# Kernel optimization log

Measured on AMD Instinct MI355X. Metric: run time of the kernel, lower is better.

## Reference

```python
import jax, jax.numpy as jnp
import numpy as np

N = 50000       # nodes
E = 800000      # edges (before self-loops)
F_IN = 128
HID = 64
HEADS = 4
OUT_DIM = 128
N_CLS = 2
NG = 500        # num graphs
SLOPE = 0.2     # GATConv leaky_relu negative slope
EPS = 1e-5      # BatchNorm eps


def setup_inputs() -> dict:
    key = jax.random.key(0)
    ks = jax.random.split(key, 24)
    s = 0.05
    d = {
        "x": jax.random.normal(ks[0], (N, F_IN), jnp.float32),
        "edge_index": jax.random.randint(ks[1], (2, E), 0, N, jnp.int64),
        "batch": jnp.sort(jax.random.randint(ks[2], (N,), 0, NG, jnp.int64)),
        # GATConv 1
        "W1": jax.random.normal(ks[3], (F_IN, HEADS * HID), jnp.float32) * s,
        "att_src1": jax.random.normal(ks[4], (HEADS, HID), jnp.float32) * s,
        "att_dst1": jax.random.normal(ks[5], (HEADS, HID), jnp.float32) * s,
        "b1": jnp.zeros((HEADS * HID,), jnp.float32),
        # BN1 (eval mode)
        "g1": jnp.ones((HEADS * HID,), jnp.float32),
        "be1": jnp.zeros((HEADS * HID,), jnp.float32),
        "rm1": jnp.zeros((HEADS * HID,), jnp.float32),
        "rv1": jnp.ones((HEADS * HID,), jnp.float32),
        # GATConv 2
        "W2": jax.random.normal(ks[6], (HEADS * HID, HEADS * HID), jnp.float32) * s,
        "att_src2": jax.random.normal(ks[7], (HEADS, HID), jnp.float32) * s,
        "att_dst2": jax.random.normal(ks[8], (HEADS, HID), jnp.float32) * s,
        "b2": jnp.zeros((HEADS * HID,), jnp.float32),
        # BN2 (eval mode)
        "g2": jnp.ones((HEADS * HID,), jnp.float32),
        "be2": jnp.zeros((HEADS * HID,), jnp.float32),
        "rm2": jnp.zeros((HEADS * HID,), jnp.float32),
        "rv2": jnp.ones((HEADS * HID,), jnp.float32),
        # MLP head
        "lw1": jax.random.normal(ks[9], (HEADS * HID, OUT_DIM), jnp.float32) * s,
        "lb1": jnp.zeros((OUT_DIM,), jnp.float32),
        "lw2": jax.random.normal(ks[10], (OUT_DIM, N_CLS), jnp.float32) * s,
        "lb2": jnp.zeros((N_CLS,), jnp.float32),
    }
    return d


def _gat_conv(x, src, dst, W, a_src, a_dst, b):
    """PyG GATConv (concat heads, add_self_loops=True, eval -> no dropout)."""
    n = x.shape[0]
    h = (x @ W).reshape(n, HEADS, -1)            # [N, H, C]
    loop = jnp.arange(n)
    s = jnp.concatenate([src, loop])             # self-loops appended
    d = jnp.concatenate([dst, loop])
    a_s = jnp.sum(h * a_src, axis=-1)            # [N, H]
    a_d = jnp.sum(h * a_dst, axis=-1)            # [N, H]
    e = jax.nn.leaky_relu(a_s[s] + a_d[d], SLOPE)   # [Et, H]
    # softmax over incoming edges per destination node
    m = jax.ops.segment_max(e, d, num_segments=n)
    ex = jnp.exp(e - m[d])
    denom = jax.ops.segment_sum(ex, d, num_segments=n)
    alpha = ex / denom[d]                        # [Et, H]
    msg = h[s] * alpha[:, :, None]               # [Et, H, C]
    out = jax.ops.segment_sum(msg, d, num_segments=n)
    return out.reshape(n, -1) + b


def _bn_eval(x, g, be, rm, rv):
    return (x - rm) * jax.lax.rsqrt(rv + EPS) * g + be


def reference(x, edge_index, batch, W1, att_src1, att_dst1, b1, g1, be1, rm1, rv1,
              W2, att_src2, att_dst2, b2, g2, be2, rm2, rv2, lw1, lb1, lw2, lb2):
    src, dst = edge_index[0], edge_index[1]
    h = jax.nn.relu(_gat_conv(x, src, dst, W1, att_src1, att_dst1, b1))
    h = _bn_eval(h, g1, be1, rm1, rv1)
    h = jax.nn.relu(_gat_conv(h, src, dst, W2, att_src2, att_dst2, b2))
    h = _bn_eval(h, g2, be2, rm2, rv2)
    # global mean pool over graphs
    sums = jax.ops.segment_sum(h, batch, num_segments=NG)
    cnt = jax.ops.segment_sum(jnp.ones((h.shape[0],), h.dtype), batch, num_segments=NG)
    pooled = sums / jnp.clip(cnt, 1.0)[:, None]
    z = jax.nn.relu(pooled @ lw1 + lb1)
    return z @ lw2 + lb2
```

## Files before the change

### kernel.cpp

```cpp
#include <hip/hip_runtime.h>
#include <hip/hip_bf16.h>
#include <math.h>

#define N_NODES 50000
#define M_PAD   50048
#define N_EDGES 800000
#define F_IN 128
#define HID 64
#define HEADS 4
#define FEAT 256
#define OUT_DIM 128
#define N_CLS 2
#define NG 500
#define SLOPE 0.2f
#define BN_EPS 1e-5f
#define WCAP 64
#define NCHUNK ((N_NODES + 255) / 256)

typedef __attribute__((ext_vector_type(8))) short short8;
typedef __attribute__((ext_vector_type(4))) float floatx4;
typedef __attribute__((ext_vector_type(2))) float floatx2;

__device__ inline unsigned short f2bf(float f) {
    unsigned int u = __float_as_uint(f);
    unsigned int lsb = (u >> 16) & 1u;
    return (unsigned short)((u + 0x7fffu + lsb) >> 16);
}

template<bool AF32>
__global__ __launch_bounds__(256) void gemm_mfma_gat(
    const void* __restrict__ Av, const unsigned short* __restrict__ BT,
    const float* __restrict__ att_src, const float* __restrict__ att_dst,
    unsigned char* __restrict__ h8, float* __restrict__ a_s,
    float* __restrict__ a_d, int K) {
    constexpr int LS = 40;
    constexpr int C8 = 144;
    __shared__ unsigned short smem[128 * 132];
    unsigned short* As = smem;
    unsigned short* Bs = smem + 128 * LS;
    unsigned char*  s8 = (unsigned char*)smem;
    int t = threadIdx.x;
    int lane = t & 63, w = t >> 6;
    int wm = (w >> 1) * 64, wn = (w & 1) * 64;
    int row0 = blockIdx.y * 128, col0 = blockIdx.x * 128;

    floatx4 acc[4][4] = {};

    int r0 = t >> 2,            c0 = (t & 3) * 8;
    int r1 = (t + 256) >> 2,    c1 = ((t + 256) & 3) * 8;
    int mrow = lane & 15, quad = lane >> 4;

    const unsigned short* Ab = (const unsigned short*)Av;
    const float* Af = (const float*)Av;

    for (int k0 = 0; k0 < K; k0 += 32) {
        if (AF32) {
            uint4 p0 = make_uint4(0, 0, 0, 0), p1 = p0;
            if (row0 + r0 < N_NODES) {
                float4 f0 = *(const float4*)&Af[(long long)(row0 + r0) * K + k0 + c0];
                float4 f1 = *(const float4*)&Af[(long long)(row0 + r0) * K + k0 + c0 + 4];
                p0.x = (unsigned)f2bf(f0.x) | ((unsigned)f2bf(f0.y) << 16);
                p0.y = (unsigned)f2bf(f0.z) | ((unsigned)f2bf(f0.w) << 16);
                p0.z = (unsigned)f2bf(f1.x) | ((unsigned)f2bf(f1.y) << 16);
                p0.w = (unsigned)f2bf(f1.z) | ((unsigned)f2bf(f1.w) << 16);
            }
            if (row0 + r1 < N_NODES) {
                float4 f0 = *(const float4*)&Af[(long long)(row0 + r1) * K + k0 + c1];
                float4 f1 = *(const float4*)&Af[(long long)(row0 + r1) * K + k0 + c1 + 4];
                p1.x = (unsigned)f2bf(f0.x) | ((unsigned)f2bf(f0.y) << 16);
                p1.y = (unsigned)f2bf(f0.z) | ((unsigned)f2bf(f0.w) << 16);
                p1.z = (unsigned)f2bf(f1.x) | ((unsigned)f2bf(f1.y) << 16);
                p1.w = (unsigned)f2bf(f1.z) | ((unsigned)f2bf(f1.w) << 16);
            }
            *(uint4*)&As[r0 * LS + c0] = p0;
            *(uint4*)&As[r1 * LS + c1] = p1;
        } else {
            *(uint4*)&As[r0 * LS + c0] = *(const uint4*)&Ab[(long long)(row0 + r0) * K + k0 + c0];
            *(uint4*)&As[r1 * LS + c1] = *(const uint4*)&Ab[(long long)(row0 + r1) * K + k0 + c1];
        }
        *(uint4*)&Bs[r0 * LS + c0] = *(const uint4*)&BT[(long long)(col0 + r0) * K + k0 + c0];
        *(uint4*)&Bs[r1 * LS + c1] = *(const uint4*)&BT[(long long)(col0 + r1) * K + k0 + c1];
        __syncthreads();
        short8 af[4], bf[4];
        #pragma unroll
        for (int i = 0; i < 4; i++) {
            af[i] = *(const short8*)&As[(wm + i * 16 + mrow) * LS + quad * 8];
            bf[i] = *(const short8*)&Bs[(wn + i * 16 + mrow) * LS + quad * 8];
        }
        #pragma unroll
        for (int mi = 0; mi < 4; mi++)
            #pragma unroll
            for (int ni = 0; ni < 4; ni++)
                acc[mi][ni] = __builtin_amdgcn_mfma_f32_16x16x32_bf16(af[mi], bf[ni],
                                                                      acc[mi][ni], 0, 0, 0);
        __syncthreads();
    }

    int head = blockIdx.x * 2 + (w & 1);
    float ats[4], atd[4];
    #pragma unroll
    for (int ni = 0; ni < 4; ni++) {
        ats[ni] = att_src[head * 64 + ni * 16 + mrow];
        atd[ni] = att_dst[head * 64 + ni * 16 + mrow];
    }
    #pragma unroll
    for (int mi = 0; mi < 4; mi++) {
        #pragma unroll
        for (int r = 0; r < 4; r++) {
            int row = row0 + wm + mi * 16 + quad * 4 + r;
            float ps = 0.f, pd = 0.f;
            #pragma unroll
            for (int ni = 0; ni < 4; ni++) {
                float v = acc[mi][ni][r];
                ps += v * ats[ni];
                pd += v * atd[ni];
            }
            #pragma unroll
            for (int off = 1; off < 16; off <<= 1) {
                ps += __shfl_xor(ps, off);
                pd += __shfl_xor(pd, off);
            }
            if (mrow == 0 && row < N_NODES) {
                a_s[row * 4 + head] = ps;
                a_d[row * 4 + head] = pd;
            }
        }
    }

    #pragma unroll
    for (int mi = 0; mi < 4; mi++)
        #pragma unroll
        for (int r = 0; r < 4; r++) {
            int row = wm + mi * 16 + quad * 4 + r;
            #pragma unroll
            for (int ni = 0; ni < 4; ni += 2) {
                int pk = __builtin_amdgcn_cvt_pk_fp8_f32(acc[mi][ni][r],
                                                         acc[mi][ni + 1][r], 0, false);
                s8[row * C8 + wn + ni * 16 + mrow]       = (unsigned char)(pk & 0xff);
                s8[row * C8 + wn + (ni + 1) * 16 + mrow] = (unsigned char)((pk >> 8) & 0xff);
            }
        }
    __syncthreads();
    {
        int r2 = t >> 1, half = t & 1;
        const uint4* sp = (const uint4*)&s8[r2 * C8 + half * 64];
        uint4* dp = (uint4*)&h8[(long long)(row0 + r2) * FEAT + col0 + half * 64];
        #pragma unroll
        for (int k = 0; k < 4; k++)
            dp[k] = sp[k];
    }
}

__global__ void prep(const float* __restrict__ W1, const float* __restrict__ W2,
                     unsigned short* __restrict__ W1T, unsigned short* __restrict__ W2T,
                     int* __restrict__ deg, unsigned long long* __restrict__ h1bf_pad) {
    int i = blockIdx.x * 256 + threadIdx.x;
    if (i < F_IN * 256) {
        int k = i >> 8, n = i & 255;
        W1T[n * F_IN + k] = f2bf(W1[i]);
    }
    int j = i - F_IN * 256;
    if (j >= 0 && j < FEAT * 256) {
        int k = j >> 8, n = j & 255;
        W2T[n * FEAT + k] = f2bf(W2[j]);
    }
    if (i < N_NODES) deg[i] = 0;
    if (i < (M_PAD - N_NODES) * FEAT / 4) h1bf_pad[i] = 0ULL;
}

__global__ void degree_count(const int* __restrict__ src, const int* __restrict__ dst,
                             int* __restrict__ deg, int* __restrict__ epos) {
    int e = blockIdx.x * blockDim.x + threadIdx.x;
    if (e >= N_EDGES + N_NODES) return;
    int d = (e < N_EDGES) ? dst[e] : (e - N_EDGES);
    epos[e] = atomicAdd(&deg[d], 1);
}

__global__ __launch_bounds__(256) void scan_k1(const int* __restrict__ deg,
                                               int* __restrict__ bsum) {
    int b = blockIdx.x, t = threadIdx.x;
    int i = b * 256 + t;
    int v = (i < N_NODES) ? deg[i] : 0;
    #pragma unroll
    for (int off = 32; off > 0; off >>= 1) v += __shfl_down(v, off);
    __shared__ int ws[4];
    if ((t & 63) == 0) ws[t >> 6] = v;
    __syncthreads();
    if (t == 0) bsum[b] = ws[0] + ws[1] + ws[2] + ws[3];
}

__global__ __launch_bounds__(256) void scan_k2(const int* __restrict__ bsum,
                                               int* __restrict__ boff,
                                               int* __restrict__ row_start) {
    int t = threadIdx.x;
    int lane = t & 63, wid = t >> 6;
    int v = (t < NCHUNK) ? bsum[t] : 0;
    int x = v;
    #pragma unroll
    for (int off = 1; off < 64; off <<= 1) {
        int y = __shfl_up(x, off);
        if (lane >= off) x += y;
    }
    __shared__ int wsum[4], woff[4];
    if (lane == 63) wsum[wid] = x;
    __syncthreads();
    if (t == 0) {
        int s = 0;
        #pragma unroll
        for (int w = 0; w < 4; w++) { int tw = wsum[w]; woff[w] = s; s += tw; }
        row_start[N_NODES] = s;
    }
    __syncthreads();
    if (t < NCHUNK) boff[t] = x - v + woff[wid];
}

__global__ __launch_bounds__(256) void scan_k3(const int* __restrict__ deg,
                                               const int* __restrict__ boff,
                                               int* __restrict__ row_start) {
    int b = blockIdx.x, t = threadIdx.x;
    int lane = t & 63, wid = t >> 6;
    int i = b * 256 + t;
    int v = (i < N_NODES) ? deg[i] : 0;
    int x = v;
    #pragma unroll
    for (int off = 1; off < 64; off <<= 1) {
        int y = __shfl_up(x, off);
        if (lane >= off) x += y;
    }
    __shared__ int wsum[4], woff[4];
    if (lane == 63) wsum[wid] = x;
    __syncthreads();
    if (t == 0) {
        int s = boff[b];
        #pragma unroll
        for (int w = 0; w < 4; w++) { int tw = wsum[w]; woff[w] = s; s += tw; }
    }
    __syncthreads();
    if (i < N_NODES) row_start[i] = x - v + woff[wid];
}

__global__ void scatter_edges(const int* __restrict__ src, const int* __restrict__ dst,
                              const int* __restrict__ row_start, const int* __restrict__ epos,
                              int* __restrict__ csr_src) {
    int e = blockIdx.x * blockDim.x + threadIdx.x;
    if (e >= N_EDGES + N_NODES) return;
    int s, d;
    if (e < N_EDGES) { s = src[e]; d = dst[e]; } else { s = d = e - N_EDGES; }
    csr_src[row_start[d] + epos[e]] = s;
}

__global__ __launch_bounds__(256) void gat_fused(
    const int* __restrict__ row_start, const int* __restrict__ csr_src,
    const float* __restrict__ a_s, const float* __restrict__ a_d,
    const unsigned char* __restrict__ h8, const float* __restrict__ bias,
    const float* __restrict__ g, const float* __restrict__ be,
    const float* __restrict__ rm, const float* __restrict__ rv,
    unsigned short* __restrict__ out16) {
    int t = threadIdx.x;
    int lane = t & 63;
    int w = t >> 6;
    int hd = lane >> 4;
    int d = blockIdx.x * 4 + w;

    __shared__ float p_lds[4 * WCAP * 4];
    __shared__ int   o_lds[4 * WCAP];
    float* pw = &p_lds[w * WCAP * 4];
    int*   ow = &o_lds[w * WCAP];

    const unsigned int* __restrict__ H1 = (const unsigned int*)h8;

    int rs = row_start[d], re = row_start[d + 1];
    int deg = re - rs;
    float4 ad4 = *(const float4*)&a_d[d * 4];

    float m_old = -INFINITY;
    float den = 0.f;
    float4 acc = make_float4(0.f, 0.f, 0.f, 0.f);

    for (int base = 0; base < deg; base += WCAP) {
        int cl = min(WCAP, deg - base);
        float lg[4] = {-INFINITY, -INFINITY, -INFINITY, -INFINITY};
        if (lane < cl) {
            int s = csr_src[rs + base + lane];
            ow[lane] = s * 64;
            float4 as4 = *(const float4*)&a_s[s * 4];
            float e0 = as4.x + ad4.x; lg[0] = e0 > 0.f ? e0 : SLOPE * e0;
            float e1 = as4.y + ad4.y; lg[1] = e1 > 0.f ? e1 : SLOPE * e1;
            float e2 = as4.z + ad4.z; lg[2] = e2 > 0.f ? e2 : SLOPE * e2;
            float e3 = as4.w + ad4.w; lg[3] = e3 > 0.f ? e3 : SLOPE * e3;
        }
        float mm = fmaxf(fmaxf(lg[0], lg[1]), fmaxf(lg[2], lg[3]));
        #pragma unroll
        for (int off = 1; off < 64; off <<= 1) mm = fmaxf(mm, __shfl_xor(mm, off));
        float m_new = fmaxf(m_old, mm);
        float alpha = __expf(m_old - m_new);
        m_old = m_new;
        if (lane < cl) {
            float4 pq;
            pq.x = __expf(lg[0] - m_new);
            pq.y = __expf(lg[1] - m_new);
            pq.z = __expf(lg[2] - m_new);
            pq.w = __expf(lg[3] - m_new);
            *(float4*)&pw[lane * 4] = pq;
        }
        acc.x *= alpha; acc.y *= alpha; acc.z *= alpha; acc.w *= alpha;
        den *= alpha;
        int e = 0;
        for (; e + 1 < cl; e += 2) {
            int oA = ow[e], oB = ow[e + 1];
            float pA = pw[e * 4 + hd], pB = pw[(e + 1) * 4 + hd];
            int uA = (int)H1[oA + lane];
            int uB = (int)H1[oB + lane];
            den += pA + pB;
            floatx2 a0 = __builtin_amdgcn_cvt_pk_f32_fp8(uA, false);
            floatx2 a1 = __builtin_amdgcn_cvt_pk_f32_fp8(uA, true);
            floatx2 b0 = __builtin_amdgcn_cvt_pk_f32_fp8(uB, false);
            floatx2 b1 = __builtin_amdgcn_cvt_pk_f32_fp8(uB, true);
            acc.x += pA * a0.x; acc.y += pA * a0.y;
            acc.z += pA * a1.x; acc.w += pA * a1.y;
            acc.x += pB * b0.x; acc.y += pB * b0.y;
            acc.z += pB * b1.x; acc.w += pB * b1.y;
        }
        if (e < cl) {
            int oA = ow[e];
            float pA = pw[e * 4 + hd];
            int uA = (int)H1[oA + lane];
            den += pA;
            floatx2 a0 = __builtin_amdgcn_cvt_pk_f32_fp8(uA, false);
            floatx2 a1 = __builtin_amdgcn_cvt_pk_f32_fp8(uA, true);
            acc.x += pA * a0.x; acc.y += pA * a0.y;
            acc.z += pA * a1.x; acc.w += pA * a1.y;
        }
    }
    float inv = 1.f / den;
    int c0 = lane * 4;
    float4 bi = *(const float4*)&bias[c0];
    float4 gg = *(const float4*)&g[c0];
    float4 bb = *(const float4*)&be[c0];
    float4 mm4 = *(const float4*)&rm[c0];
    float4 vv = *(const float4*)&rv[c0];
    float v0 = fmaxf(acc.x * inv + bi.x, 0.f);
    float v1 = fmaxf(acc.y * inv + bi.y, 0.f);
    float v2 = fmaxf(acc.z * inv + bi.z, 0.f);
    float v3 = fmaxf(acc.w * inv + bi.w, 0.f);
    v0 = (v0 - mm4.x) * rsqrtf(vv.x + BN_EPS) * gg.x + bb.x;
    v1 = (v1 - mm4.y) * rsqrtf(vv.y + BN_EPS) * gg.y + bb.y;
    v2 = (v2 - mm4.z) * rsqrtf(vv.z + BN_EPS) * gg.z + bb.z;
    v3 = (v3 - mm4.w) * rsqrtf(vv.w + BN_EPS) * gg.w + bb.w;
    unsigned long long o =
        (unsigned long long)f2bf(v0) |
        ((unsigned long long)f2bf(v1) << 16) |
        ((unsigned long long)f2bf(v2) << 32) |
        ((unsigned long long)f2bf(v3) << 48);
    __builtin_nontemporal_store(o, (unsigned long long*)&out16[(long long)d * FEAT + c0]);
}

__global__ __launch_bounds__(256) void head_fused(
    const unsigned short* __restrict__ h2, const int* __restrict__ batch,
    const float* __restrict__ lw1, const float* __restrict__ lb1,
    const float* __restrict__ lw2, const float* __restrict__ lb2,
    float* __restrict__ out) {
    int gph = blockIdx.x;
    int t = threadIdx.x;
    __shared__ float pooled[FEAT];
    __shared__ float zl[OUT_DIM];
    __shared__ int lo_s, hi_s;
    if (t == 0) {
        int lo = 0, hi = N_NODES;
        while (lo < hi) { int mid = (lo + hi) >> 1; if (batch[mid] < gph) lo = mid + 1; else hi = mid; }
        lo_s = lo;
        int lo2 = 0, hi2 = N_NODES;
        while (lo2 < hi2) { int mid = (lo2 + hi2) >> 1; if (batch[mid] < gph + 1) lo2 = mid + 1; else hi2 = mid; }
        hi_s = lo2;
    }
    __syncthreads();
    int lo = lo_s, hi = hi_s;
    float a0 = 0.f, a1 = 0.f, a2 = 0.f, a3 = 0.f;
    int n = lo;
    for (; n + 3 < hi; n += 4) {
        a0 += __uint_as_float((unsigned)h2[(long long)n * FEAT + t] << 16);
        a1 += __uint_as_float((unsigned)h2[(long long)(n + 1) * FEAT + t] << 16);
        a2 += __uint_as_float((unsigned)h2[(long long)(n + 2) * FEAT + t] << 16);
        a3 += __uint_as_float((unsigned)h2[(long long)(n + 3) * FEAT + t] << 16);
    }
    for (; n < hi; n++) a0 += __uint_as_float((unsigned)h2[(long long)n * FEAT + t] << 16);
    float cnt = fmaxf((float)(hi - lo), 1.f);
    pooled[t] = (a0 + a1 + a2 + a3) / cnt;
    __syncthreads();
    int j = t >> 1, kh = t & 1;
    float zp = 0.f;
    #pragma unroll 8
    for (int k = kh * 128; k < kh * 128 + 128; k++)
        zp += pooled[k] * lw1[k * OUT_DIM + j];
    zp += __shfl_xor(zp, 1);
    if (kh == 0) zl[j] = fmaxf(zp + lb1[j], 0.f);
    __syncthreads();
    int w = t >> 6, lane = t & 63;
    if (w < 2) {
        float p = zl[lane] * lw2[lane * 2 + w] + zl[lane + 64] * lw2[(lane + 64) * 2 + w];
        #pragma unroll
        for (int off = 1; off < 64; off <<= 1) p += __shfl_xor(p, off);
        if (lane == 0) out[gph * 2 + w] = p + lb2[w];
    }
}

extern "C" void kernel_launch(void* const* d_in, const int* in_sizes, int n_in,
                              void* d_out, int out_size, void* d_ws, size_t ws_size,
                              hipStream_t stream) {
    const float* x       = (const float*)d_in[0];
    const int*   ei      = (const int*)d_in[1];
    const int*   batch   = (const int*)d_in[2];
    const float* W1      = (const float*)d_in[3];
    const float* att_s1  = (const float*)d_in[4];
    const float* att_d1  = (const float*)d_in[5];
    const float* b1      = (const float*)d_in[6];
    const float* g1      = (const float*)d_in[7];
    const float* be1     = (const float*)d_in[8];
    const float* rm1     = (const float*)d_in[9];
    const float* rv1     = (const float*)d_in[10];
    const float* W2      = (const float*)d_in[11];
    const float* att_s2  = (const float*)d_in[12];
    const float* att_d2  = (const float*)d_in[13];
    const float* b2      = (const float*)d_in[14];
    const float* g2      = (const float*)d_in[15];
    const float* be2     = (const float*)d_in[16];
    const float* rm2     = (const float*)d_in[17];
    const float* rv2     = (const float*)d_in[18];
    const float* lw1     = (const float*)d_in[19];
    const float* lb1     = (const float*)d_in[20];
    const float* lw2     = (const float*)d_in[21];
    const float* lb2     = (const float*)d_in[22];
    float* out           = (float*)d_out;

    const int* src = ei;
    const int* dst = ei + N_EDGES;

    char* p = (char*)d_ws;
    auto carve = [&p](size_t bytes) -> void* {
        void* r = (void*)p;
        p += (bytes + 63) & ~(size_t)63;
        return r;
    };
    unsigned short* h2bf = (unsigned short*)carve(sizeof(short) * (size_t)N_NODES * FEAT);
    float* a_s    = (float*)carve(sizeof(float) * N_NODES * HEADS);
    float* a_d    = (float*)carve(sizeof(float) * N_NODES * HEADS);
    int*   deg    = (int*)carve(sizeof(int) * N_NODES);
    int*   epos   = (int*)carve(sizeof(int) * (N_EDGES + N_NODES));
    int*   csr    = (int*)carve(sizeof(int) * (N_EDGES + N_NODES));
    int*   rstart = (int*)carve(sizeof(int) * (N_NODES + 4));
    int*   bsum   = (int*)carve(sizeof(int) * 256);
    int*   boff   = (int*)carve(sizeof(int) * 256);
    unsigned char*  h8   = (unsigned char*)carve((size_t)M_PAD * FEAT);
    unsigned short* h1bf = (unsigned short*)carve(sizeof(short) * (size_t)M_PAD * FEAT);
    unsigned short* w1t  = (unsigned short*)carve(sizeof(short) * FEAT * F_IN);
    unsigned short* w2t  = (unsigned short*)carve(sizeof(short) * FEAT * FEAT);

    const int Et = N_EDGES + N_NODES;

    prep<<<((F_IN + FEAT) * 256 + 255) / 256, 256, 0, stream>>>(
        W1, W2, w1t, w2t, deg,
        (unsigned long long*)(h1bf + (size_t)N_NODES * FEAT));

    degree_count<<<(Et + 255) / 256, 256, 0, stream>>>(src, dst, deg, epos);
    scan_k1<<<NCHUNK, 256, 0, stream>>>(deg, bsum);
    scan_k2<<<1, 256, 0, stream>>>(bsum, boff, rstart);
    scan_k3<<<NCHUNK, 256, 0, stream>>>(deg, boff, rstart);
    scatter_edges<<<(Et + 255) / 256, 256, 0, stream>>>(src, dst, rstart, epos, csr);

    {
        dim3 grid(FEAT / 128, M_PAD / 128);
        gemm_mfma_gat<true><<<grid, 256, 0, stream>>>(x, w1t, att_s1, att_d1,
                                                      h8, a_s, a_d, F_IN);
    }
    gat_fused<<<N_NODES / 4, 256, 0, stream>>>(rstart, csr, a_s, a_d, h8,
                                               b1, g1, be1, rm1, rv1, h1bf);

    {
        dim3 grid(FEAT / 128, M_PAD / 128);
        gemm_mfma_gat<false><<<grid, 256, 0, stream>>>(h1bf, w2t, att_s2, att_d2,
                                                       h8, a_s, a_d, FEAT);
    }
    gat_fused<<<N_NODES / 4, 256, 0, stream>>>(rstart, csr, a_s, a_d, h8,
                                               b2, g2, be2, rm2, rv2, h2bf);

    head_fused<<<NG, 256, 0, stream>>>(h2bf, batch, lw1, lb1, lw2, lb2, out);
}
```

Measured before the change: 354.4 us.

## Widen GEMM tile to full 256 columns per block and add single-chunk softmax path

```diff
diff --git a/kernel.cpp b/kernel.cpp
--- a/kernel.cpp
+++ b/kernel.cpp
@@ -28,86 +28,80 @@
 }
 
 template<bool AF32>
-__global__ __launch_bounds__(256) void gemm_mfma_gat(
+__global__ __launch_bounds__(256, 2) void gemm_mfma_gat(
     const void* __restrict__ Av, const unsigned short* __restrict__ BT,
     const float* __restrict__ att_src, const float* __restrict__ att_dst,
     unsigned char* __restrict__ h8, float* __restrict__ a_s,
     float* __restrict__ a_d, int K) {
     constexpr int LS = 40;
-    constexpr int C8 = 144;
-    __shared__ unsigned short smem[128 * 132];
-    unsigned short* As = smem;
-    unsigned short* Bs = smem + 128 * LS;
-    unsigned char*  s8 = (unsigned char*)smem;
+    constexpr int C8 = 272;
+    __shared__ __align__(16) unsigned char smem_raw[128 * C8];
+    unsigned short* As = (unsigned short*)smem_raw;
+    unsigned short* Bs = As + 128 * LS;
+    unsigned char*  s8 = smem_raw;
     int t = threadIdx.x;
     int lane = t & 63, w = t >> 6;
-    int wm = (w >> 1) * 64, wn = (w & 1) * 64;
-    int row0 = blockIdx.y * 128, col0 = blockIdx.x * 128;
-
-    floatx4 acc[4][4] = {};
-
-    int r0 = t >> 2,            c0 = (t & 3) * 8;
-    int r1 = (t + 256) >> 2,    c1 = ((t + 256) & 3) * 8;
+    int row0 = blockIdx.x * 128;
     int mrow = lane & 15, quad = lane >> 4;
+
+    floatx4 acc[8][4] = {};
+
+    int rA = t >> 2, cA = (t & 3) * 8;
 
     const unsigned short* Ab = (const unsigned short*)Av;
     const float* Af = (const float*)Av;
 
     for (int k0 = 0; k0 < K; k0 += 32) {
-        if (AF32) {
-            uint4 p0 = make_uint4(0, 0, 0, 0), p1 = p0;
-            if (row0 + r0 < N_NODES) {
-                float4 f0 = *(const float4*)&Af[(long long)(row0 + r0) * K + k0 + c0];
-                float4 f1 = *(const float4*)&Af[(long long)(row0 + r0) * K + k0 + c0 + 4];
-                p0.x = (unsigned)f2bf(f0.x) | ((unsigned)f2bf(f0.y) << 16);
-                p0.y = (unsigned)f2bf(f0.z) | ((unsigned)f2bf(f0.w) << 16);
-                p0.z = (unsigned)f2bf(f1.x) | ((unsigned)f2bf(f1.y) << 16);
-                p0.w = (unsigned)f2bf(f1.z) | ((unsigned)f2bf(f1.w) << 16);
-            }
-            if (row0 + r1 < N_NODES) {
-                float4 f0 = *(const float4*)&Af[(long long)(row0 + r1) * K + k0 + c1];
-                float4 f1 = *(const float4*)&Af[(long long)(row0 + r1) * K + k0 + c1 + 4];
-                p1.x = (unsigned)f2bf(f0.x) | ((unsigned)f2bf(f0.y) << 16);
-                p1.y = (unsigned)f2bf(f0.z) | ((unsigned)f2bf(f0.w) << 16);
-                p1.z = (unsigned)f2bf(f1.x) | ((unsigned)f2bf(f1.y) << 16);
-                p1.w = (unsigned)f2bf(f1.z) | ((unsigned)f2bf(f1.w) << 16);
-            }
-            *(uint4*)&As[r0 * LS + c0] = p0;
-            *(uint4*)&As[r1 * LS + c1] = p1;
-        } else {
-            *(uint4*)&As[r0 * LS + c0] = *(const uint4*)&Ab[(long long)(row0 + r0) * K + k0 + c0];
-            *(uint4*)&As[r1 * LS + c1] = *(const uint4*)&Ab[(long long)(row0 + r1) * K + k0 + c1];
-        }
-        *(uint4*)&Bs[r0 * LS + c0] = *(const uint4*)&BT[(long long)(col0 + r0) * K + k0 + c0];
-        *(uint4*)&Bs[r1 * LS + c1] = *(const uint4*)&BT[(long long)(col0 + r1) * K + k0 + c1];
+        #pragma unroll
+        for (int j = 0; j < 2; j++) {
+            int r = rA + j * 64;
+            if (AF32) {
+                uint4 pk = make_uint4(0, 0, 0, 0);
+                if (row0 + r < N_NODES) {
+                    float4 f0 = *(const float4*)&Af[(long long)(row0 + r) * K + k0 + cA];
+                    float4 f1 = *(const float4*)&Af[(long long)(row0 + r) * K + k0 + cA + 4];
+                    pk.x = (unsigned)f2bf(f0.x) | ((unsigned)f2bf(f0.y) << 16);
+                    pk.y = (unsigned)f2bf(f0.z) | ((unsigned)f2bf(f0.w) << 16);
+                    pk.z = (unsigned)f2bf(f1.x) | ((unsigned)f2bf(f1.y) << 16);
+                    pk.w = (unsigned)f2bf(f1.z) | ((unsigned)f2bf(f1.w) << 16);
+                }
+                *(uint4*)&As[r * LS + cA] = pk;
+            } else {
+                *(uint4*)&As[r * LS + cA] = *(const uint4*)&Ab[(long long)(row0 + r) * K + k0 + cA];
+            }
+        }
+        #pragma unroll
+        for (int j = 0; j < 4; j++) {
+            int r = rA + j * 64;
+            *(uint4*)&Bs[r * LS + cA] = *(const uint4*)&BT[(long long)r * K + k0 + cA];
+        }
         __syncthreads();
-        short8 af[4], bf[4];
-        #pragma unroll
-        for (int i = 0; i < 4; i++) {
-            af[i] = *(const short8*)&As[(wm + i * 16 + mrow) * LS + quad * 8];
-            bf[i] = *(const short8*)&Bs[(wn + i * 16 + mrow) * LS + quad * 8];
-        }
-        #pragma unroll
-        for (int mi = 0; mi < 4; mi++)
+        short8 bf[4];
+        #pragma unroll
+        for (int ni = 0; ni < 4; ni++)
+            bf[ni] = *(const short8*)&Bs[(w * 64 + ni * 16 + mrow) * LS + quad * 8];
+        #pragma unroll
+        for (int mi = 0; mi < 8; mi++) {
+            short8 af = *(const short8*)&As[(mi * 16 + mrow) * LS + quad * 8];
             #pragma unroll
             for (int ni = 0; ni < 4; ni++)
-                acc[mi][ni] = __builtin_amdgcn_mfma_f32_16x16x32_bf16(af[mi], bf[ni],
+                acc[mi][ni] = __builtin_amdgcn_mfma_f32_16x16x32_bf16(af, bf[ni],
                                                                       acc[mi][ni], 0, 0, 0);
+        }
         __syncthreads();
     }
 
-    int head = blockIdx.x * 2 + (w & 1);
     float ats[4], atd[4];
     #pragma unroll
     for (int ni = 0; ni < 4; ni++) {
-        ats[ni] = att_src[head * 64 + ni * 16 + mrow];
-        atd[ni] = att_dst[head * 64 + ni * 16 + mrow];
+        ats[ni] = att_src[w * 64 + ni * 16 + mrow];
+        atd[ni] = att_dst[w * 64 + ni * 16 + mrow];
     }
     #pragma unroll
-    for (int mi = 0; mi < 4; mi++) {
+    for (int mi = 0; mi < 8; mi++) {
         #pragma unroll
         for (int r = 0; r < 4; r++) {
-            int row = row0 + wm + mi * 16 + quad * 4 + r;
+            int row = row0 + mi * 16 + quad * 4 + r;
             float ps = 0.f, pd = 0.f;
             #pragma unroll
             for (int ni = 0; ni < 4; ni++) {
@@ -121,32 +115,32 @@
                 pd += __shfl_xor(pd, off);
             }
             if (mrow == 0 && row < N_NODES) {
-                a_s[row * 4 + head] = ps;
-                a_d[row * 4 + head] = pd;
+                a_s[row * 4 + w] = ps;
+                a_d[row * 4 + w] = pd;
             }
         }
     }
 
     #pragma unroll
-    for (int mi = 0; mi < 4; mi++)
+    for (int mi = 0; mi < 8; mi++)
         #pragma unroll
         for (int r = 0; r < 4; r++) {
-            int row = wm + mi * 16 + quad * 4 + r;
+            int row = mi * 16 + quad * 4 + r;
             #pragma unroll
             for (int ni = 0; ni < 4; ni += 2) {
                 int pk = __builtin_amdgcn_cvt_pk_fp8_f32(acc[mi][ni][r],
                                                          acc[mi][ni + 1][r], 0, false);
-                s8[row * C8 + wn + ni * 16 + mrow]       = (unsigned char)(pk & 0xff);
-                s8[row * C8 + wn + (ni + 1) * 16 + mrow] = (unsigned char)((pk >> 8) & 0xff);
+                s8[row * C8 + w * 64 + ni * 16 + mrow]       = (unsigned char)(pk & 0xff);
+                s8[row * C8 + w * 64 + (ni + 1) * 16 + mrow] = (unsigned char)((pk >> 8) & 0xff);
             }
         }
     __syncthreads();
     {
         int r2 = t >> 1, half = t & 1;
-        const uint4* sp = (const uint4*)&s8[r2 * C8 + half * 64];
-        uint4* dp = (uint4*)&h8[(long long)(row0 + r2) * FEAT + col0 + half * 64];
-        #pragma unroll
-        for (int k = 0; k < 4; k++)
+        const uint4* sp = (const uint4*)&s8[r2 * C8 + half * 128];
+        uint4* dp = (uint4*)&h8[(long long)(row0 + r2) * FEAT + half * 128];
+        #pragma unroll
+        for (int k = 0; k < 8; k++)
             dp[k] = sp[k];
     }
 }
@@ -273,15 +267,13 @@
     int deg = re - rs;
     float4 ad4 = *(const float4*)&a_d[d * 4];
 
-    float m_old = -INFINITY;
     float den = 0.f;
     float4 acc = make_float4(0.f, 0.f, 0.f, 0.f);
 
-    for (int base = 0; base < deg; base += WCAP) {
-        int cl = min(WCAP, deg - base);
+    if (deg <= WCAP) {
         float lg[4] = {-INFINITY, -INFINITY, -INFINITY, -INFINITY};
-        if (lane < cl) {
-            int s = csr_src[rs + base + lane];
+        if (lane < deg) {
+            int s = csr_src[rs + lane];
             ow[lane] = s * 64;
             float4 as4 = *(const float4*)&a_s[s * 4];
             float e0 = as4.x + ad4.x; lg[0] = e0 > 0.f ? e0 : SLOPE * e0;
@@ -292,21 +284,16 @@
         float mm = fmaxf(fmaxf(lg[0], lg[1]), fmaxf(lg[2], lg[3]));
         #pragma unroll
         for (int off = 1; off < 64; off <<= 1) mm = fmaxf(mm, __shfl_xor(mm, off));
-        float m_new = fmaxf(m_old, mm);
-        float alpha = __expf(m_old - m_new);
-        m_old = m_new;
-        if (lane < cl) {
+        if (lane < deg) {
             float4 pq;
-            pq.x = __expf(lg[0] - m_new);
-            pq.y = __expf(lg[1] - m_new);
-            pq.z = __expf(lg[2] - m_new);
-            pq.w = __expf(lg[3] - m_new);
+            pq.x = __expf(lg[0] - mm);
+            pq.y = __expf(lg[1] - mm);
+            pq.z = __expf(lg[2] - mm);
+            pq.w = __expf(lg[3] - mm);
             *(float4*)&pw[lane * 4] = pq;
         }
-        acc.x *= alpha; acc.y *= alpha; acc.z *= alpha; acc.w *= alpha;
-        den *= alpha;
         int e = 0;
-        for (; e + 1 < cl; e += 2) {
+        for (; e + 1 < deg; e += 2) {
             int oA = ow[e], oB = ow[e + 1];
             float pA = pw[e * 4 + hd], pB = pw[(e + 1) * 4 + hd];
             int uA = (int)H1[oA + lane];
@@ -321,7 +308,7 @@
             acc.x += pB * b0.x; acc.y += pB * b0.y;
             acc.z += pB * b1.x; acc.w += pB * b1.y;
         }
-        if (e < cl) {
+        if (e < deg) {
             int oA = ow[e];
             float pA = pw[e * 4 + hd];
             int uA = (int)H1[oA + lane];
@@ -330,6 +317,63 @@
             floatx2 a1 = __builtin_amdgcn_cvt_pk_f32_fp8(uA, true);
             acc.x += pA * a0.x; acc.y += pA * a0.y;
             acc.z += pA * a1.x; acc.w += pA * a1.y;
+        }
+    } else {
+        float m_old = -INFINITY;
+        for (int base = 0; base < deg; base += WCAP) {
+            int cl = min(WCAP, deg - base);
+            float lg[4] = {-INFINITY, -INFINITY, -INFINITY, -INFINITY};
+            if (lane < cl) {
+                int s = csr_src[rs + base + lane];
+                ow[lane] = s * 64;
+                float4 as4 = *(const float4*)&a_s[s * 4];
+                float e0 = as4.x + ad4.x; lg[0] = e0 > 0.f ? e0 : SLOPE * e0;
+                float e1 = as4.y + ad4.y; lg[1] = e1 > 0.f ? e1 : SLOPE * e1;
+                float e2 = as4.z + ad4.z; lg[2] = e2 > 0.f ? e2 : SLOPE * e2;
+                float e3 = as4.w + ad4.w; lg[3] = e3 > 0.f ? e3 : SLOPE * e3;
+            }
+            float mm = fmaxf(fmaxf(lg[0], lg[1]), fmaxf(lg[2], lg[3]));
+            #pragma unroll
+            for (int off = 1; off < 64; off <<= 1) mm = fmaxf(mm, __shfl_xor(mm, off));
+            float m_new = fmaxf(m_old, mm);
+            float alpha = __expf(m_old - m_new);
+            m_old = m_new;
+            if (lane < cl) {
+                float4 pq;
+                pq.x = __expf(lg[0] - m_new);
+                pq.y = __expf(lg[1] - m_new);
+                pq.z = __expf(lg[2] - m_new);
+                pq.w = __expf(lg[3] - m_new);
+                *(float4*)&pw[lane * 4] = pq;
+            }
+            acc.x *= alpha; acc.y *= alpha; acc.z *= alpha; acc.w *= alpha;
+            den *= alpha;
+            int e = 0;
+            for (; e + 1 < cl; e += 2) {
+                int oA = ow[e], oB = ow[e + 1];
+                float pA = pw[e * 4 + hd], pB = pw[(e + 1) * 4 + hd];
+                int uA = (int)H1[oA + lane];
+                int uB = (int)H1[oB + lane];
+                den += pA + pB;
+                floatx2 a0 = __builtin_amdgcn_cvt_pk_f32_fp8(uA, false);
+                floatx2 a1 = __builtin_amdgcn_cvt_pk_f32_fp8(uA, true);
+                floatx2 b0 = __builtin_amdgcn_cvt_pk_f32_fp8(uB, false);
+                floatx2 b1 = __builtin_amdgcn_cvt_pk_f32_fp8(uB, true);
+                acc.x += pA * a0.x; acc.y += pA * a0.y;
+                acc.z += pA * a1.x; acc.w += pA * a1.y;
+                acc.x += pB * b0.x; acc.y += pB * b0.y;
+                acc.z += pB * b1.x; acc.w += pB * b1.y;
+            }
+            if (e < cl) {
+                int oA = ow[e];
+                float pA = pw[e * 4 + hd];
+                int uA = (int)H1[oA + lane];
+                den += pA;
+                floatx2 a0 = __builtin_amdgcn_cvt_pk_f32_fp8(uA, false);
+                floatx2 a1 = __builtin_amdgcn_cvt_pk_f32_fp8(uA, true);
+                acc.x += pA * a0.x; acc.y += pA * a0.y;
+                acc.z += pA * a1.x; acc.w += pA * a1.y;
+            }
         }
     }
     float inv = 1.f / den;
@@ -467,19 +511,13 @@
     scan_k3<<<NCHUNK, 256, 0, stream>>>(deg, boff, rstart);
     scatter_edges<<<(Et + 255) / 256, 256, 0, stream>>>(src, dst, rstart, epos, csr);
 
-    {
-        dim3 grid(FEAT / 128, M_PAD / 128);
-        gemm_mfma_gat<true><<<grid, 256, 0, stream>>>(x, w1t, att_s1, att_d1,
-                                                      h8, a_s, a_d, F_IN);
-    }
+    gemm_mfma_gat<true><<<M_PAD / 128, 256, 0, stream>>>(x, w1t, att_s1, att_d1,
+                                                         h8, a_s, a_d, F_IN);
     gat_fused<<<N_NODES / 4, 256, 0, stream>>>(rstart, csr, a_s, a_d, h8,
                                                b1, g1, be1, rm1, rv1, h1bf);
 
-    {
-        dim3 grid(FEAT / 128, M_PAD / 128);
-        gemm_mfma_gat<false><<<grid, 256, 0, stream>>>(h1bf, w2t, att_s2, att_d2,
-                                                       h8, a_s, a_d, FEAT);
-    }
+    gemm_mfma_gat<false><<<M_PAD / 128, 256, 0, stream>>>(h1bf, w2t, att_s2, att_d2,
+                                                          h8, a_s, a_d, FEAT);
     gat_fused<<<N_NODES / 4, 256, 0, stream>>>(rstart, csr, a_s, a_d, h8,
                                                b2, g2, be2, rm2, rv2, h2bf);
 
```

New measurement: 339.9 us. 1.04x faster.
